# Optimization experiments

Measured on AMD Instinct MI355X. Metric: run time of the kernel, lower is better.

Reference implementation:

```python
import jax, jax.numpy as jnp
import numpy as np

N_EXPERTS = 8
D_MODEL = 1024
D_FF = 2048
NUM_TOKENS = 16384


def setup_inputs() -> dict:
    key = jax.random.key(0)
    k1, k2, k3, k4 = jax.random.split(key, 4)
    x = jax.random.normal(k1, (NUM_TOKENS, D_MODEL), dtype=jnp.float32)
    expert_indices = jax.random.randint(k2, (NUM_TOKENS,), 0, N_EXPERTS, dtype=jnp.int32)
    # init per nn.init.normal_(std=0.02)
    gate_up_weight = 0.02 * jax.random.normal(k3, (N_EXPERTS, 2 * D_FF, D_MODEL), dtype=jnp.float32)
    down_weight = 0.02 * jax.random.normal(k4, (N_EXPERTS, D_MODEL, D_FF), dtype=jnp.float32)
    return {"x": x, "expert_indices": expert_indices,
            "gate_up_weight": gate_up_weight, "down_weight": down_weight}


def reference(x, expert_indices, gate_up_weight, down_weight):
    # Faithful math: each token t uses expert e = expert_indices[t]:
    #   combined = x @ gate_up_weight[e].T ; gate, up = split ; h = silu(gate)*up
    #   out = h @ down_weight[e].T
    # Implemented as a fixed loop over the (small) expert set with masked
    # accumulation, avoiding the original's per-token [2F,D] weight gather.
    n_experts = gate_up_weight.shape[0]
    d_ff = down_weight.shape[2]
    out = jnp.zeros((x.shape[0], down_weight.shape[1]), dtype=x.dtype)
    for e in range(n_experts):
        combined = x @ gate_up_weight[e].T                  # [T, 2*d_ff]
        gate, up = combined[:, :d_ff], combined[:, d_ff:]
        hidden = jax.nn.silu(gate) * up                     # [T, d_ff]
        o = hidden @ down_weight[e].T                       # [T, d_model]
        out = out + jnp.where((expert_indices == e)[:, None], o, 0.0)
    return out
```

## Files before the change

kernel.cpp:

```cpp
#include <hip/hip_runtime.h>

#define NTOK 16384
#define DM 1024
#define DFF 2048
#define NE 8

typedef unsigned short u16;
typedef __attribute__((ext_vector_type(8))) short bf16x8;
typedef __attribute__((ext_vector_type(4))) float f32x4;

__device__ __forceinline__ u16 f2bf(float f) {
  unsigned u = __float_as_uint(f);
  u += 0x7fff + ((u >> 16) & 1);
  return (u16)(u >> 16);
}

__device__ __forceinline__ void async16(const void* g, void* l) {
  __builtin_amdgcn_global_load_lds(
      (const __attribute__((address_space(1))) unsigned int*)g,
      (__attribute__((address_space(3))) unsigned int*)l, 16, 0, 0);
}

__global__ void k_count(const int* __restrict__ idx, int* __restrict__ counts) {
  int t = blockIdx.x * 256 + threadIdx.x;
  atomicAdd(&counts[idx[t]], 1);
}

__global__ void k_offsets(int* __restrict__ c) {
  if (threadIdx.x == 0) {
    int acc = 0;
    for (int e = 0; e < NE; e++) { c[8 + e] = acc; c[16 + e] = acc; acc += c[e]; }
  }
}

__global__ void k_scatter(const int* __restrict__ idx, int* __restrict__ cursor,
                          int* __restrict__ tl) {
  int t = blockIdx.x * 256 + threadIdx.x;
  int pos = atomicAdd(&cursor[idx[t]], 1);
  tl[pos] = t;
}

__global__ void k_cvt_all(const float* __restrict__ x, const float* __restrict__ wgu,
                          const float* __restrict__ wd, u16* __restrict__ xb,
                          u16* __restrict__ wgub, u16* __restrict__ wdb) {
  const size_t N1 = (size_t)NTOK * DM;
  const size_t N2 = (size_t)NE * 2 * DFF * DM;
  const size_t N3 = (size_t)NE * DM * DFF;
  const size_t total4 = (N1 + N2 + N3) / 4;
  for (size_t q = (size_t)blockIdx.x * 256 + threadIdx.x; q < total4;
       q += (size_t)gridDim.x * 256) {
    size_t i = q * 4;
    const float* s;
    u16* d;
    if (i < N1) { s = x + i; d = xb + i; }
    else if (i < N1 + N2) { s = wgu + (i - N1); d = wgub + (i - N1); }
    else { s = wd + (i - N1 - N2); d = wdb + (i - N1 - N2); }
    float4 v = *(const float4*)s;
    ushort4 o;
    o.x = f2bf(v.x); o.y = f2bf(v.y); o.z = f2bf(v.z); o.w = f2bf(v.w);
    *(ushort4*)d = o;
  }
}

__global__ __launch_bounds__(512, 2) void k_gemm1(
    const u16* __restrict__ xb, const u16* __restrict__ wgu,
    u16* __restrict__ hid, const int* __restrict__ tl,
    const int* __restrict__ offs, const int* __restrict__ counts) {
  int wg = blockIdx.x;
  int e = wg & 7;
  int r = wg >> 3;
  int bx = r % 9;
  int by = r / 9;
  int Me = counts[e];
  int m0 = bx * 256;
  if (m0 >= Me) return;
  int n0 = by * 128;
  int oe = offs[e];
  const int* tle = tl + oe;

  int tid = threadIdx.x;
  int lane = tid & 63;
  int wid = tid >> 6;
  int wm = wid >> 2;
  int wn = wid & 3;

  __shared__ u16 lds[2][2][256 * 64];

  int lr = lane >> 3;
  int swz = ((lane & 7) ^ lr) * 8;
  const u16* pA[4];
  const u16* pB[4];
#pragma unroll
  for (int j = 0; j < 4; j++) {
    int c = j * 8 + wid;
    int a = m0 + c * 8 + lr;
    if (a >= Me) a = Me - 1;
    pA[j] = xb + (size_t)tle[a] * DM + swz;
    int b = c * 8 + lr;
    int grow = ((b >> 5) & 1) * DFF + n0 + ((b >> 6) & 3) * 32 + (b & 31);
    pB[j] = wgu + ((size_t)e * 2 * DFF + grow) * DM + swz;
  }

  f32x4 acc[8][4];
#pragma unroll
  for (int m = 0; m < 8; m++)
#pragma unroll
    for (int f = 0; f < 4; f++) acc[m][f] = (f32x4){0.f, 0.f, 0.f, 0.f};

  const int r15 = lane & 15;
  const int hi4 = lane >> 4;
  const int rx = r15 & 7;

#pragma unroll
  for (int j = 0; j < 4; j++) {
    int off = (j * 8 + wid) * 1024;
    async16(pA[j], (char*)&lds[0][0][0] + off);
    async16(pB[j], (char*)&lds[0][1][0] + off);
  }
  asm volatile("s_waitcnt vmcnt(0)" ::: "memory");
  __builtin_amdgcn_s_barrier();
  __builtin_amdgcn_sched_barrier(0);

  int cur = 0;
#pragma unroll 1
  for (int t = 0; t < DM / 64; t++) {
    const char* Ab = (const char*)&lds[cur][0][0];
    const char* Bb = (const char*)&lds[cur][1][0];
    char* LA = (char*)&lds[cur ^ 1][0][0];
    char* LB = (char*)&lds[cur ^ 1][1][0];
    int k1 = (t + 1) * 64;
    bool pf = (t < DM / 64 - 1);
    bf16x8 bfr[4][2];
#pragma unroll
    for (int p = 0; p < 4; p++) {
      if (p == 0) {
#pragma unroll
        for (int f = 0; f < 4; f++)
#pragma unroll
          for (int kk = 0; kk < 2; kk++) {
            int row = wn * 64 + f * 16 + r15;
            bfr[f][kk] = *(const bf16x8*)(Bb + row * 128 + (((kk * 4 + hi4) ^ rx) * 16));
          }
      }
      bf16x8 af[2][2];
#pragma unroll
      for (int i = 0; i < 2; i++)
#pragma unroll
        for (int kk = 0; kk < 2; kk++) {
          int row = wm * 128 + (2 * p + i) * 16 + r15;
          af[i][kk] = *(const bf16x8*)(Ab + row * 128 + (((kk * 4 + hi4) ^ rx) * 16));
        }
      if (pf && p < 2) {
#pragma unroll
        for (int j = 0; j < 2; j++) {
          int jj = p * 2 + j;
          int off = (jj * 8 + wid) * 1024;
          async16(pA[jj] + k1, LA + off);
          async16(pB[jj] + k1, LB + off);
        }
      }
      __builtin_amdgcn_s_barrier();
      __builtin_amdgcn_sched_barrier(0);
      __builtin_amdgcn_s_setprio(1);
#pragma unroll
      for (int kk = 0; kk < 2; kk++)
#pragma unroll
        for (int i = 0; i < 2; i++)
#pragma unroll
          for (int f = 0; f < 4; f++)
            acc[2 * p + i][f] = __builtin_amdgcn_mfma_f32_16x16x32_bf16(
                af[i][kk], bfr[f][kk], acc[2 * p + i][f], 0, 0, 0);
      __builtin_amdgcn_s_setprio(0);
      __builtin_amdgcn_sched_barrier(0);
    }
    asm volatile("s_waitcnt vmcnt(0)" ::: "memory");
    __builtin_amdgcn_s_barrier();
    __builtin_amdgcn_sched_barrier(0);
    cur ^= 1;
  }

  int colb = n0 + wn * 32 + r15;
#pragma unroll
  for (int m = 0; m < 8; m++) {
#pragma unroll
    for (int rr = 0; rr < 4; rr++) {
      int gm = m0 + wm * 128 + m * 16 + hi4 * 4 + rr;
      if (gm < Me) {
        size_t rowp = (size_t)(oe + gm) * DFF;
#pragma unroll
        for (int f = 0; f < 2; f++) {
          float g = acc[m][f][rr];
          float u = acc[m][f + 2][rr];
          float s = g / (1.0f + __expf(-g));
          hid[rowp + colb + f * 16] = f2bf(s * u);
        }
      }
    }
  }
}

__global__ __launch_bounds__(256, 2) void k_gemm2(
    const u16* __restrict__ hid, const u16* __restrict__ wd,
    float* __restrict__ out, const int* __restrict__ tl,
    const int* __restrict__ offs, const int* __restrict__ counts) {
  int wg = blockIdx.x;
  int e = wg & 7;
  int r = wg >> 3;
  int bx = r % 17;
  int by = r / 17;
  int Me = counts[e];
  int m0 = bx * 128;
  if (m0 >= Me) return;
  int n0 = by * 128;
  int oe = offs[e];
  const int* tle = tl + oe;

  int tid = threadIdx.x;
  int lane = tid & 63;
  int wid = tid >> 6;
  int wm = wid >> 1;
  int wn = wid & 1;

  __shared__ u16 lds[2][2][128 * 64];

  int lr = lane >> 3;
  int swz = ((lane & 7) ^ lr) * 8;
  const u16* pA[4];
  const u16* pB[4];
#pragma unroll
  for (int j = 0; j < 4; j++) {
    int c = j * 4 + wid;
    int a = m0 + c * 8 + lr;
    if (a >= Me) a = Me - 1;
    pA[j] = hid + (size_t)(oe + a) * DFF + swz;
    pB[j] = wd + ((size_t)e * DM + n0 + c * 8 + lr) * DFF + swz;
  }

  f32x4 acc[4][4];
#pragma unroll
  for (int m = 0; m < 4; m++)
#pragma unroll
    for (int f = 0; f < 4; f++) acc[m][f] = (f32x4){0.f, 0.f, 0.f, 0.f};

  const int r15 = lane & 15;
  const int hi4 = lane >> 4;
  const int rx = r15 & 7;

#pragma unroll
  for (int j = 0; j < 4; j++) {
    int off = (j * 4 + wid) * 1024;
    async16(pA[j], (char*)&lds[0][0][0] + off);
    async16(pB[j], (char*)&lds[0][1][0] + off);
  }
  asm volatile("s_waitcnt vmcnt(0)" ::: "memory");
  __builtin_amdgcn_s_barrier();
  __builtin_amdgcn_sched_barrier(0);

  int cur = 0;
#pragma unroll 1
  for (int t = 0; t < DFF / 64; t++) {
    const char* Ab = (const char*)&lds[cur][0][0];
    const char* Bb = (const char*)&lds[cur][1][0];
    char* LA = (char*)&lds[cur ^ 1][0][0];
    char* LB = (char*)&lds[cur ^ 1][1][0];
    int k1 = (t + 1) * 64;
    bool pf = (t < DFF / 64 - 1);
    bf16x8 bfr[4][2];
#pragma unroll
    for (int p = 0; p < 2; p++) {
      if (p == 0) {
#pragma unroll
        for (int f = 0; f < 4; f++)
#pragma unroll
          for (int kk = 0; kk < 2; kk++) {
            int row = wn * 64 + f * 16 + r15;
            bfr[f][kk] = *(const bf16x8*)(Bb + row * 128 + (((kk * 4 + hi4) ^ rx) * 16));
          }
      }
      bf16x8 af[2][2];
#pragma unroll
      for (int i = 0; i < 2; i++)
#pragma unroll
        for (int kk = 0; kk < 2; kk++) {
          int row = wm * 64 + (2 * p + i) * 16 + r15;
          af[i][kk] = *(const bf16x8*)(Ab + row * 128 + (((kk * 4 + hi4) ^ rx) * 16));
        }
      if (pf) {
#pragma unroll
        for (int j = 0; j < 2; j++) {
          int jj = p * 2 + j;
          int off = (jj * 4 + wid) * 1024;
          async16(pA[jj] + k1, LA + off);
          async16(pB[jj] + k1, LB + off);
        }
      }
      __builtin_amdgcn_s_barrier();
      __builtin_amdgcn_sched_barrier(0);
      __builtin_amdgcn_s_setprio(1);
#pragma unroll
      for (int kk = 0; kk < 2; kk++)
#pragma unroll
        for (int i = 0; i < 2; i++)
#pragma unroll
          for (int f = 0; f < 4; f++)
            acc[2 * p + i][f] = __builtin_amdgcn_mfma_f32_16x16x32_bf16(
                af[i][kk], bfr[f][kk], acc[2 * p + i][f], 0, 0, 0);
      __builtin_amdgcn_s_setprio(0);
      __builtin_amdgcn_sched_barrier(0);
    }
    asm volatile("s_waitcnt vmcnt(0)" ::: "memory");
    __builtin_amdgcn_s_barrier();
    __builtin_amdgcn_sched_barrier(0);
    cur ^= 1;
  }

  int colb = n0 + wn * 64 + r15;
#pragma unroll
  for (int m = 0; m < 4; m++) {
#pragma unroll
    for (int rr = 0; rr < 4; rr++) {
      int gm = m0 + wm * 64 + m * 16 + hi4 * 4 + rr;
      if (gm < Me) {
        int tk = tle[gm];
#pragma unroll
        for (int f = 0; f < 4; f++)
          out[(size_t)tk * DM + colb + f * 16] = acc[m][f][rr];
      }
    }
  }
}

extern "C" void kernel_launch(void* const* d_in, const int* in_sizes, int n_in,
                              void* d_out, int out_size, void* d_ws, size_t ws_size,
                              hipStream_t stream) {
  const float* x   = (const float*)d_in[0];
  const int* eidx  = (const int*)d_in[1];
  const float* wgu = (const float*)d_in[2];
  const float* wd  = (const float*)d_in[3];
  float* out = (float*)d_out;
  char* ws = (char*)d_ws;

  int* ctrl = (int*)ws;
  int* toklist = (int*)(ws + 256);
  u16* xb   = (u16*)(ws + 65792);
  u16* wgub = (u16*)(ws + 65792 + 33554432ull);
  u16* wdb  = (u16*)(ws + 65792 + 33554432ull + 67108864ull);
  u16* hid  = (u16*)(ws + 65792 + 33554432ull + 67108864ull + 33554432ull);

  hipMemsetAsync(ws, 0, 256, stream);
  k_count<<<NTOK / 256, 256, 0, stream>>>(eidx, ctrl);
  k_offsets<<<1, 64, 0, stream>>>(ctrl);
  k_scatter<<<NTOK / 256, 256, 0, stream>>>(eidx, ctrl + 16, toklist);

  k_cvt_all<<<2048, 256, 0, stream>>>(x, wgu, wd, xb, wgub, wdb);

  k_gemm1<<<9 * 16 * NE, 512, 0, stream>>>(xb, wgub, hid, toklist, ctrl + 8, ctrl);
  k_gemm2<<<17 * 8 * NE, 256, 0, stream>>>(hid, wdb, out, toklist, ctrl + 8, ctrl);
}
```

Baseline: 478.7 us.

## Switch both grouped GEMMs to triple-buffered K=32 tiles with two-stage prefetch

Both expert GEMM kernels move from double-buffered 64-wide K tiles to triple-buffered 32-wide K tiles. Loads are issued two iterations ahead and waited on with a partial vmcnt, so global-to-LDS latency overlaps more compute. The LDS swizzle is redone for 64-byte rows. gemm2's launch bounds rise to 3 waves per SIMD, since its smaller LDS footprint may allow more occupancy. The cost is twice as many loop iterations and barriers per tile, plus some register pressure from the higher occupancy target.

Measured after the change: 472.6 us. No clear change (-1.3%).

```diff
diff --git a/kernel.cpp b/kernel.cpp
--- a/kernel.cpp
+++ b/kernel.cpp
@@ -84,21 +84,21 @@
   int wm = wid >> 2;
   int wn = wid & 3;
 
-  __shared__ u16 lds[2][2][256 * 64];
-
-  int lr = lane >> 3;
-  int swz = ((lane & 7) ^ lr) * 8;
-  const u16* pA[4];
-  const u16* pB[4];
-#pragma unroll
-  for (int j = 0; j < 4; j++) {
+  __shared__ u16 lds[3][2][256 * 32];
+
+  int lrc = lane >> 2;
+  int sw = ((lane & 3) ^ ((lane >> 3) & 3)) * 8;
+  const u16* pA[2];
+  const u16* pB[2];
+#pragma unroll
+  for (int j = 0; j < 2; j++) {
     int c = j * 8 + wid;
-    int a = m0 + c * 8 + lr;
+    int a = m0 + c * 16 + lrc;
     if (a >= Me) a = Me - 1;
-    pA[j] = xb + (size_t)tle[a] * DM + swz;
-    int b = c * 8 + lr;
+    pA[j] = xb + (size_t)tle[a] * DM + sw;
+    int b = c * 16 + lrc;
     int grow = ((b >> 5) & 1) * DFF + n0 + ((b >> 6) & 3) * 32 + (b & 31);
-    pB[j] = wgu + ((size_t)e * 2 * DFF + grow) * DM + swz;
+    pB[j] = wgu + ((size_t)e * 2 * DFF + grow) * DM + sw;
   }
 
   f32x4 acc[8][4];
@@ -109,74 +109,79 @@
 
   const int r15 = lane & 15;
   const int hi4 = lane >> 4;
-  const int rx = r15 & 7;
-
-#pragma unroll
-  for (int j = 0; j < 4; j++) {
+  const int slotb = (hi4 ^ ((r15 >> 1) & 3)) * 16;
+
+  char* A0 = (char*)&lds[0][0][0]; char* B0 = (char*)&lds[0][1][0];
+  char* A1 = (char*)&lds[1][0][0]; char* B1 = (char*)&lds[1][1][0];
+  char* A2 = (char*)&lds[2][0][0]; char* B2 = (char*)&lds[2][1][0];
+
+  const int NT = DM / 32;
+
+#pragma unroll
+  for (int j = 0; j < 2; j++) {
     int off = (j * 8 + wid) * 1024;
-    async16(pA[j], (char*)&lds[0][0][0] + off);
-    async16(pB[j], (char*)&lds[0][1][0] + off);
-  }
-  asm volatile("s_waitcnt vmcnt(0)" ::: "memory");
+    async16(pA[j], A0 + off);
+    async16(pB[j], B0 + off);
+  }
+#pragma unroll
+  for (int j = 0; j < 2; j++) {
+    int off = (j * 8 + wid) * 1024;
+    async16(pA[j] + 32, A1 + off);
+    async16(pB[j] + 32, B1 + off);
+  }
+  asm volatile("s_waitcnt vmcnt(4)" ::: "memory");
   __builtin_amdgcn_s_barrier();
   __builtin_amdgcn_sched_barrier(0);
 
-  int cur = 0;
 #pragma unroll 1
-  for (int t = 0; t < DM / 64; t++) {
-    const char* Ab = (const char*)&lds[cur][0][0];
-    const char* Bb = (const char*)&lds[cur][1][0];
-    char* LA = (char*)&lds[cur ^ 1][0][0];
-    char* LB = (char*)&lds[cur ^ 1][1][0];
-    int k1 = (t + 1) * 64;
-    bool pf = (t < DM / 64 - 1);
-    bf16x8 bfr[4][2];
-#pragma unroll
-    for (int p = 0; p < 4; p++) {
+  for (int t = 0; t < NT; t++) {
+    int k2 = (t + 2) * 32;
+    bool deep = (t + 2 < NT);
+    bf16x8 bfr[4];
+#pragma unroll
+    for (int p = 0; p < 2; p++) {
       if (p == 0) {
 #pragma unroll
-        for (int f = 0; f < 4; f++)
-#pragma unroll
-          for (int kk = 0; kk < 2; kk++) {
-            int row = wn * 64 + f * 16 + r15;
-            bfr[f][kk] = *(const bf16x8*)(Bb + row * 128 + (((kk * 4 + hi4) ^ rx) * 16));
-          }
-      }
-      bf16x8 af[2][2];
-#pragma unroll
-      for (int i = 0; i < 2; i++)
-#pragma unroll
-        for (int kk = 0; kk < 2; kk++) {
-          int row = wm * 128 + (2 * p + i) * 16 + r15;
-          af[i][kk] = *(const bf16x8*)(Ab + row * 128 + (((kk * 4 + hi4) ^ rx) * 16));
-        }
-      if (pf && p < 2) {
-#pragma unroll
-        for (int j = 0; j < 2; j++) {
-          int jj = p * 2 + j;
-          int off = (jj * 8 + wid) * 1024;
-          async16(pA[jj] + k1, LA + off);
-          async16(pB[jj] + k1, LB + off);
+        for (int f = 0; f < 4; f++) {
+          int row = wn * 64 + f * 16 + r15;
+          bfr[f] = *(const bf16x8*)(B0 + row * 64 + slotb);
+        }
+      }
+      bf16x8 af[4];
+#pragma unroll
+      for (int i = 0; i < 4; i++) {
+        int row = wm * 128 + (p * 4 + i) * 16 + r15;
+        af[i] = *(const bf16x8*)(A0 + row * 64 + slotb);
+      }
+      if (deep) {
+        if (p == 0) {
+#pragma unroll
+          for (int j = 0; j < 2; j++)
+            async16(pA[j] + k2, A2 + (j * 8 + wid) * 1024);
+        } else {
+#pragma unroll
+          for (int j = 0; j < 2; j++)
+            async16(pB[j] + k2, B2 + (j * 8 + wid) * 1024);
         }
       }
       __builtin_amdgcn_s_barrier();
       __builtin_amdgcn_sched_barrier(0);
       __builtin_amdgcn_s_setprio(1);
 #pragma unroll
-      for (int kk = 0; kk < 2; kk++)
-#pragma unroll
-        for (int i = 0; i < 2; i++)
-#pragma unroll
-          for (int f = 0; f < 4; f++)
-            acc[2 * p + i][f] = __builtin_amdgcn_mfma_f32_16x16x32_bf16(
-                af[i][kk], bfr[f][kk], acc[2 * p + i][f], 0, 0, 0);
+      for (int i = 0; i < 4; i++)
+#pragma unroll
+        for (int f = 0; f < 4; f++)
+          acc[p * 4 + i][f] = __builtin_amdgcn_mfma_f32_16x16x32_bf16(
+              af[i], bfr[f], acc[p * 4 + i][f], 0, 0, 0);
       __builtin_amdgcn_s_setprio(0);
       __builtin_amdgcn_sched_barrier(0);
     }
-    asm volatile("s_waitcnt vmcnt(0)" ::: "memory");
+    if (deep) { asm volatile("s_waitcnt vmcnt(4)" ::: "memory"); }
+    else      { asm volatile("s_waitcnt vmcnt(0)" ::: "memory"); }
     __builtin_amdgcn_s_barrier();
     __builtin_amdgcn_sched_barrier(0);
-    cur ^= 1;
+    char* tA = A0; A0 = A1; A1 = A2; A2 = tA;
+    char* tB = B0; B0 = B1; B1 = B2; B2 = tB;
   }
 
   int colb = n0 + wn * 32 + r15;
@@ -199,7 +204,7 @@
   }
 }
 
-__global__ __launch_bounds__(256, 2) void k_gemm2(
+__global__ __launch_bounds__(256, 3) void k_gemm2(
     const u16* __restrict__ hid, const u16* __restrict__ wd,
     float* __restrict__ out, const int* __restrict__ tl,
     const int* __restrict__ offs, const int* __restrict__ counts) {
@@ -221,19 +226,19 @@
   int wm = wid >> 1;
   int wn = wid & 1;
 
-  __shared__ u16 lds[2][2][128 * 64];
-
-  int lr = lane >> 3;
-  int swz = ((lane & 7) ^ lr) * 8;
-  const u16* pA[4];
-  const u16* pB[4];
-#pragma unroll
-  for (int j = 0; j < 4; j++) {
+  __shared__ u16 lds[3][2][128 * 32];
+
+  int lrc = lane >> 2;
+  int sw = ((lane & 3) ^ ((lane >> 3) & 3)) * 8;
+  const u16* pA[2];
+  const u16* pB[2];
+#pragma unroll
+  for (int j = 0; j < 2; j++) {
     int c = j * 4 + wid;
-    int a = m0 + c * 8 + lr;
+    int a = m0 + c * 16 + lrc;
     if (a >= Me) a = Me - 1;
-    pA[j] = hid + (size_t)(oe + a) * DFF + swz;
-    pB[j] = wd + ((size_t)e * DM + n0 + c * 8 + lr) * DFF + swz;
+    pA[j] = hid + (size_t)(oe + a) * DFF + sw;
+    pB[j] = wd + ((size_t)e * DM + n0 + c * 16 + lrc) * DFF + sw;
   }
 
   f32x4 acc[4][4];
@@ -244,74 +249,79 @@
 
   const int r15 = lane & 15;
   const int hi4 = lane >> 4;
-  const int rx = r15 & 7;
-
-#pragma unroll
-  for (int j = 0; j < 4; j++) {
+  const int slotb = (hi4 ^ ((r15 >> 1) & 3)) * 16;
+
+  char* A0 = (char*)&lds[0][0][0]; char* B0 = (char*)&lds[0][1][0];
+  char* A1 = (char*)&lds[1][0][0]; char* B1 = (char*)&lds[1][1][0];
+  char* A2 = (char*)&lds[2][0][0]; char* B2 = (char*)&lds[2][1][0];
+
+  const int NT = DFF / 32;
+
+#pragma unroll
+  for (int j = 0; j < 2; j++) {
     int off = (j * 4 + wid) * 1024;
-    async16(pA[j], (char*)&lds[0][0][0] + off);
-    async16(pB[j], (char*)&lds[0][1][0] + off);
-  }
-  asm volatile("s_waitcnt vmcnt(0)" ::: "memory");
+    async16(pA[j], A0 + off);
+    async16(pB[j], B0 + off);
+  }
+#pragma unroll
+  for (int j = 0; j < 2; j++) {
+    int off = (j * 4 + wid) * 1024;
+    async16(pA[j] + 32, A1 + off);
+    async16(pB[j] + 32, B1 + off);
+  }
+  asm volatile("s_waitcnt vmcnt(4)" ::: "memory");
   __builtin_amdgcn_s_barrier();
   __builtin_amdgcn_sched_barrier(0);
 
-  int cur = 0;
 #pragma unroll 1
-  for (int t = 0; t < DFF / 64; t++) {
-    const char* Ab = (const char*)&lds[cur][0][0];
-    const char* Bb = (const char*)&lds[cur][1][0];
-    char* LA = (char*)&lds[cur ^ 1][0][0];
-    char* LB = (char*)&lds[cur ^ 1][1][0];
-    int k1 = (t + 1) * 64;
-    bool pf = (t < DFF / 64 - 1);
-    bf16x8 bfr[4][2];
+  for (int t = 0; t < NT; t++) {
+    int k2 = (t + 2) * 32;
+    bool deep = (t + 2 < NT);
+    bf16x8 bfr[4];
 #pragma unroll
     for (int p = 0; p < 2; p++) {
       if (p == 0) {
 #pragma unroll
-        for (int f = 0; f < 4; f++)
-#pragma unroll
-          for (int kk = 0; kk < 2; kk++) {
-            int row = wn * 64 + f * 16 + r15;
-            bfr[f][kk] = *(const bf16x8*)(Bb + row * 128 + (((kk * 4 + hi4) ^ rx) * 16));
-          }
-      }
-      bf16x8 af[2][2];
-#pragma unroll
-      for (int i = 0; i < 2; i++)
-#pragma unroll
-        for (int kk = 0; kk < 2; kk++) {
-          int row = wm * 64 + (2 * p + i) * 16 + r15;
-          af[i][kk] = *(const bf16x8*)(Ab + row * 128 + (((kk * 4 + hi4) ^ rx) * 16));
-        }
-      if (pf) {
-#pragma unroll
-        for (int j = 0; j < 2; j++) {
-          int jj = p * 2 + j;
-          int off = (jj * 4 + wid) * 1024;
-          async16(pA[jj] + k1, LA + off);
-          async16(pB[jj] + k1, LB + off);
+        for (int f = 0; f < 4; f++) {
+          int row = wn * 64 + f * 16 + r15;
+          bfr[f] = *(const bf16x8*)(B0 + row * 64 + slotb);
+        }
+      }
+      bf16x8 af[2];
+#pragma unroll
+      for (int i = 0; i < 2; i++) {
+        int row = wm * 64 + (p * 2 + i) * 16 + r15;
+        af[i] = *(const bf16x8*)(A0 + row * 64 + slotb);
+      }
+      if (deep) {
+        if (p == 0) {
+#pragma unroll
+          for (int j = 0; j < 2; j++)
+            async16(pA[j] + k2, A2 + (j * 4 + wid) * 1024);
+        } else {
+#pragma unroll
+          for (int j = 0; j < 2; j++)
+            async16(pB[j] + k2, B2 + (j * 4 + wid) * 1024);
         }
       }
       __builtin_amdgcn_s_barrier();
       __builtin_amdgcn_sched_barrier(0);
       __builtin_amdgcn_s_setprio(1);
 #pragma unroll
-      for (int kk = 0; kk < 2; kk++)
-#pragma unroll
-        for (int i = 0; i < 2; i++)
-#pragma unroll
-          for (int f = 0; f < 4; f++)
-            acc[2 * p + i][f] = __builtin_amdgcn_mfma_f32_16x16x32_bf16(
-                af[i][kk], bfr[f][kk], acc[2 * p + i][f], 0, 0, 0);
+      for (int i = 0; i < 2; i++)
+#pragma unroll
+        for (int f = 0; f < 4; f++)
+          acc[p * 2 + i][f] = __builtin_amdgcn_mfma_f32_16x16x32_bf16(
+              af[i], bfr[f], acc[p * 2 + i][f], 0, 0, 0);
       __builtin_amdgcn_s_setprio(0);
       __builtin_amdgcn_sched_barrier(0);
     }
-    asm volatile("s_waitcnt vmcnt(0)" ::: "memory");
+    if (deep) { asm volatile("s_waitcnt vmcnt(4)" ::: "memory"); }
+    else      { asm volatile("s_waitcnt vmcnt(0)" ::: "memory"); }
     __builtin_amdgcn_s_barrier();
     __builtin_amdgcn_sched_barrier(0);
-    cur ^= 1;
+    char* tA = A0; A0 = A1; A1 = A2; A2 = tA;
+    char* tB = B0; B0 = B1; B1 = B2; B2 = tB;
   }
 
   int colb = n0 + wn * 64 + r15;
```

## Fuse down-weight bf16 conversion into gemm2 with deeper K pipelining

Applied to the files above, without the earlier changes.

Removes the separate fp32->bf16 conversion of the down-projection weights and instead loads fp32 weights directly in gemm2, converting them in registers before writing to LDS. The K tile shrinks to 32 with a three-stage A buffer and register-staged B prefetch two tiles ahead. This saves a full read/write pass over the down weights, but gemm2 now reads twice as many bytes per weight tile and does extra VALU conversion work per tile. Rounding changes to round-half-up for these weights.

Result: slower. 530.7 us (+10.9%).

```diff
diff --git a/kernel.cpp b/kernel.cpp
--- a/kernel.cpp
+++ b/kernel.cpp
@@ -13,6 +13,21 @@
   unsigned u = __float_as_uint(f);
   u += 0x7fff + ((u >> 16) & 1);
   return (u16)(u >> 16);
+}
+
+__device__ __forceinline__ unsigned pack2(float a, float b) {
+  unsigned ua = __float_as_uint(a) + 0x8000u;
+  unsigned ub = __float_as_uint(b) + 0x8000u;
+  return (ua >> 16) | (ub & 0xffff0000u);
+}
+
+__device__ __forceinline__ bf16x8 cvt8(const float4& a, const float4& b) {
+  union { unsigned u[4]; bf16x8 v; } r;
+  r.u[0] = pack2(a.x, a.y);
+  r.u[1] = pack2(a.z, a.w);
+  r.u[2] = pack2(b.x, b.y);
+  r.u[3] = pack2(b.z, b.w);
+  return r.v;
 }
 
 __device__ __forceinline__ void async16(const void* g, void* l) {
@@ -41,20 +56,17 @@
 }
 
 __global__ void k_cvt_all(const float* __restrict__ x, const float* __restrict__ wgu,
-                          const float* __restrict__ wd, u16* __restrict__ xb,
-                          u16* __restrict__ wgub, u16* __restrict__ wdb) {
+                          u16* __restrict__ xb, u16* __restrict__ wgub) {
   const size_t N1 = (size_t)NTOK * DM;
   const size_t N2 = (size_t)NE * 2 * DFF * DM;
-  const size_t N3 = (size_t)NE * DM * DFF;
-  const size_t total4 = (N1 + N2 + N3) / 4;
+  const size_t total4 = (N1 + N2) / 4;
   for (size_t q = (size_t)blockIdx.x * 256 + threadIdx.x; q < total4;
        q += (size_t)gridDim.x * 256) {
     size_t i = q * 4;
     const float* s;
     u16* d;
     if (i < N1) { s = x + i; d = xb + i; }
-    else if (i < N1 + N2) { s = wgu + (i - N1); d = wgub + (i - N1); }
-    else { s = wd + (i - N1 - N2); d = wdb + (i - N1 - N2); }
+    else { s = wgu + (i - N1); d = wgub + (i - N1); }
     float4 v = *(const float4*)s;
     ushort4 o;
     o.x = f2bf(v.x); o.y = f2bf(v.y); o.z = f2bf(v.z); o.w = f2bf(v.w);
@@ -200,7 +212,7 @@
 }
 
 __global__ __launch_bounds__(256, 2) void k_gemm2(
-    const u16* __restrict__ hid, const u16* __restrict__ wd,
+    const u16* __restrict__ hid, const float* __restrict__ wd,
     float* __restrict__ out, const int* __restrict__ tl,
     const int* __restrict__ offs, const int* __restrict__ counts) {
   int wg = blockIdx.x;
@@ -221,20 +233,22 @@
   int wm = wid >> 1;
   int wn = wid & 1;
 
-  __shared__ u16 lds[2][2][128 * 64];
-
-  int lr = lane >> 3;
-  int swz = ((lane & 7) ^ lr) * 8;
-  const u16* pA[4];
-  const u16* pB[4];
-#pragma unroll
-  for (int j = 0; j < 4; j++) {
+  __shared__ u16 ldsA[3][128 * 32];
+  __shared__ u16 ldsB[2][128 * 32];
+
+  int lrc = lane >> 2;
+  int sw = ((lane & 3) ^ ((lane >> 3) & 3)) * 8;
+  const u16* pA[2];
+  const float* pBw[2];
+#pragma unroll
+  for (int j = 0; j < 2; j++) {
     int c = j * 4 + wid;
-    int a = m0 + c * 8 + lr;
+    int a = m0 + c * 16 + lrc;
     if (a >= Me) a = Me - 1;
-    pA[j] = hid + (size_t)(oe + a) * DFF + swz;
-    pB[j] = wd + ((size_t)e * DM + n0 + c * 8 + lr) * DFF + swz;
-  }
+    pA[j] = hid + (size_t)(oe + a) * DFF + sw;
+    pBw[j] = wd + ((size_t)e * DM + n0 + c * 16 + lrc) * DFF + (lane & 3) * 8;
+  }
+  const int wroff = lrc * 64 + (((lane & 3) ^ ((lane >> 3) & 3)) * 16);
 
   f32x4 acc[4][4];
 #pragma unroll
@@ -244,75 +258,111 @@
 
   const int r15 = lane & 15;
   const int hi4 = lane >> 4;
-  const int rx = r15 & 7;
-
-#pragma unroll
-  for (int j = 0; j < 4; j++) {
-    int off = (j * 4 + wid) * 1024;
-    async16(pA[j], (char*)&lds[0][0][0] + off);
-    async16(pB[j], (char*)&lds[0][1][0] + off);
-  }
-  asm volatile("s_waitcnt vmcnt(0)" ::: "memory");
+  const int slotb = (hi4 ^ ((r15 >> 1) & 3)) * 16;
+
+  char* A0 = (char*)&ldsA[0][0];
+  char* A1 = (char*)&ldsA[1][0];
+  char* A2 = (char*)&ldsA[2][0];
+  char* Bc = (char*)&ldsB[0][0];
+  char* Bn = (char*)&ldsB[1][0];
+
+  const int NT = DFF / 32;
+  float4 bA[4], bB[4];
+
+#pragma unroll
+  for (int j = 0; j < 2; j++) async16(pA[j], A0 + (j * 4 + wid) * 1024);
+#pragma unroll
+  for (int j = 0; j < 2; j++) {
+    bA[2 * j] = *(const float4*)(pBw[j]);
+    bA[2 * j + 1] = *(const float4*)(pBw[j] + 4);
+  }
+#pragma unroll
+  for (int j = 0; j < 2; j++) async16(pA[j] + 32, A1 + (j * 4 + wid) * 1024);
+#pragma unroll
+  for (int j = 0; j < 2; j++) {
+    bB[2 * j] = *(const float4*)(pBw[j] + 32);
+    bB[2 * j + 1] = *(const float4*)(pBw[j] + 36);
+  }
+  asm volatile("s_waitcnt vmcnt(6)" ::: "memory");
+#pragma unroll
+  for (int j = 0; j < 2; j++)
+    *(bf16x8*)(Bc + (j * 4 + wid) * 1024 + wroff) = cvt8(bA[2 * j], bA[2 * j + 1]);
+  asm volatile("s_waitcnt lgkmcnt(0)" ::: "memory");
   __builtin_amdgcn_s_barrier();
   __builtin_amdgcn_sched_barrier(0);
 
-  int cur = 0;
+#define G2_TILE(T, BI, BW)                                                     \
+  {                                                                            \
+    int t = (T);                                                               \
+    int k2 = (t + 2) * 32;                                                     \
+    bool deep = (t + 2 < NT);                                                  \
+    bf16x8 bfr[4];                                                             \
+    _Pragma("unroll")                                                          \
+    for (int f = 0; f < 4; f++) {                                              \
+      int row = wn * 64 + f * 16 + r15;                                        \
+      bfr[f] = *(const bf16x8*)(Bc + row * 64 + slotb);                        \
+    }                                                                          \
+    bf16x8 af0[2];                                                             \
+    _Pragma("unroll")                                                          \
+    for (int i = 0; i < 2; i++) {                                              \
+      int row = wm * 64 + i * 16 + r15;                                        \
+      af0[i] = *(const bf16x8*)(A0 + row * 64 + slotb);                        \
+    }                                                                          \
+    if (deep) {                                                                \
+      _Pragma("unroll")                                                        \
+      for (int j = 0; j < 2; j++) async16(pA[j] + k2, A2 + (j * 4 + wid) * 1024); \
+      _Pragma("unroll")                                                        \
+      for (int j = 0; j < 2; j++) {                                            \
+        BI[2 * j] = *(const float4*)(pBw[j] + k2);                             \
+        BI[2 * j + 1] = *(const float4*)(pBw[j] + k2 + 4);                     \
+      }                                                                        \
+    }                                                                          \
+    __builtin_amdgcn_s_barrier();                                              \
+    __builtin_amdgcn_sched_barrier(0);                                         \
+    __builtin_amdgcn_s_setprio(1);                                             \
+    _Pragma("unroll")                                                          \
+    for (int i = 0; i < 2; i++)                                                \
+      _Pragma("unroll")                                                        \
+      for (int f = 0; f < 4; f++)                                              \
+        acc[i][f] = __builtin_amdgcn_mfma_f32_16x16x32_bf16(af0[i], bfr[f], acc[i][f], 0, 0, 0); \
+    __builtin_amdgcn_s_setprio(0);                                             \
+    __builtin_amdgcn_sched_barrier(0);                                         \
+    bf16x8 af1[2];                                                             \
+    _Pragma("unroll")                                                          \
+    for (int i = 0; i < 2; i++) {                                              \
+      int row = wm * 64 + (2 + i) * 16 + r15;                                  \
+      af1[i] = *(const bf16x8*)(A0 + row * 64 + slotb);                        \
+    }                                                                          \
+    if (deep) { asm volatile("s_waitcnt vmcnt(6)" ::: "memory"); }             \
+    else      { asm volatile("s_waitcnt vmcnt(0)" ::: "memory"); }             \
+    if (t + 1 < NT) {                                                          \
+      _Pragma("unroll")                                                        \
+      for (int j = 0; j < 2; j++)                                              \
+        *(bf16x8*)(Bn + (j * 4 + wid) * 1024 + wroff) = cvt8(BW[2 * j], BW[2 * j + 1]); \
+    }                                                                          \
+    __builtin_amdgcn_s_barrier();                                              \
+    __builtin_amdgcn_sched_barrier(0);                                         \
+    __builtin_amdgcn_s_setprio(1);                                             \
+    _Pragma("unroll")                                                          \
+    for (int i = 0; i < 2; i++)                                                \
+      _Pragma("unroll")                                                        \
+      for (int f = 0; f < 4; f++)                                              \
+        acc[2 + i][f] = __builtin_amdgcn_mfma_f32_16x16x32_bf16(af1[i], bfr[f], acc[2 + i][f], 0, 0, 0); \
+    __builtin_amdgcn_s_setprio(0);                                             \
+    __builtin_amdgcn_sched_barrier(0);                                         \
+    asm volatile("s_waitcnt lgkmcnt(0)" ::: "memory");                         \
+    __builtin_amdgcn_s_barrier();                                              \
+    __builtin_amdgcn_sched_barrier(0);                                         \
+    char* tA = A0; A0 = A1; A1 = A2; A2 = tA;                                  \
+    char* tB = Bc; Bc = Bn; Bn = tB;                                           \
+  }
+
 #pragma unroll 1
-  for (int t = 0; t < DFF / 64; t++) {
-    const char* Ab = (const char*)&lds[cur][0][0];
-    const char* Bb = (const char*)&lds[cur][1][0];
-    char* LA = (char*)&lds[cur ^ 1][0][0];
-    char* LB = (char*)&lds[cur ^ 1][1][0];
-    int k1 = (t + 1) * 64;
-    bool pf = (t < DFF / 64 - 1);
-    bf16x8 bfr[4][2];
-#pragma unroll
-    for (int p = 0; p < 2; p++) {
-      if (p == 0) {
-#pragma unroll
-        for (int f = 0; f < 4; f++)
-#pragma unroll
-          for (int kk = 0; kk < 2; kk++) {
-            int row = wn * 64 + f * 16 + r15;
-            bfr[f][kk] = *(const bf16x8*)(Bb + row * 128 + (((kk * 4 + hi4) ^ rx) * 16));
-          }
-      }
-      bf16x8 af[2][2];
-#pragma unroll
-      for (int i = 0; i < 2; i++)
-#pragma unroll
-        for (int kk = 0; kk < 2; kk++) {
-          int row = wm * 64 + (2 * p + i) * 16 + r15;
-          af[i][kk] = *(const bf16x8*)(Ab + row * 128 + (((kk * 4 + hi4) ^ rx) * 16));
-        }
-      if (pf) {
-#pragma unroll
-        for (int j = 0; j < 2; j++) {
-          int jj = p * 2 + j;
-          int off = (jj * 4 + wid) * 1024;
-          async16(pA[jj] + k1, LA + off);
-          async16(pB[jj] + k1, LB + off);
-        }
-      }
-      __builtin_amdgcn_s_barrier();
-      __builtin_amdgcn_sched_barrier(0);
-      __builtin_amdgcn_s_setprio(1);
-#pragma unroll
-      for (int kk = 0; kk < 2; kk++)
-#pragma unroll
-        for (int i = 0; i < 2; i++)
-#pragma unroll
-          for (int f = 0; f < 4; f++)
-            acc[2 * p + i][f] = __builtin_amdgcn_mfma_f32_16x16x32_bf16(
-                af[i][kk], bfr[f][kk], acc[2 * p + i][f], 0, 0, 0);
-      __builtin_amdgcn_s_setprio(0);
-      __builtin_amdgcn_sched_barrier(0);
-    }
-    asm volatile("s_waitcnt vmcnt(0)" ::: "memory");
-    __builtin_amdgcn_s_barrier();
-    __builtin_amdgcn_sched_barrier(0);
-    cur ^= 1;
-  }
+  for (int tt = 0; tt < NT; tt += 2) {
+    G2_TILE(tt, bA, bB);
+    G2_TILE(tt + 1, bB, bA);
+  }
+#undef G2_TILE
 
   int colb = n0 + wn * 64 + r15;
 #pragma unroll
@@ -344,16 +394,15 @@
   int* toklist = (int*)(ws + 256);
   u16* xb   = (u16*)(ws + 65792);
   u16* wgub = (u16*)(ws + 65792 + 33554432ull);
-  u16* wdb  = (u16*)(ws + 65792 + 33554432ull + 67108864ull);
-  u16* hid  = (u16*)(ws + 65792 + 33554432ull + 67108864ull + 33554432ull);
+  u16* hid  = (u16*)(ws + 65792 + 33554432ull + 67108864ull);
 
   hipMemsetAsync(ws, 0, 256, stream);
   k_count<<<NTOK / 256, 256, 0, stream>>>(eidx, ctrl);
   k_offsets<<<1, 64, 0, stream>>>(ctrl);
   k_scatter<<<NTOK / 256, 256, 0, stream>>>(eidx, ctrl + 16, toklist);
 
-  k_cvt_all<<<2048, 256, 0, stream>>>(x, wgu, wd, xb, wgub, wdb);
+  k_cvt_all<<<2048, 256, 0, stream>>>(x, wgu, xb, wgub);
 
   k_gemm1<<<9 * 16 * NE, 512, 0, stream>>>(xb, wgub, hid, toklist, ctrl + 8, ctrl);
-  k_gemm2<<<17 * 8 * NE, 256, 0, stream>>>(hid, wdb, out, toklist, ctrl + 8, ctrl);
-}
+  k_gemm2<<<17 * 8 * NE, 256, 0, stream>>>(hid, wd, out, toklist, ctrl + 8, ctrl);
+}
```
